# Performance work log

Hardware: AMD Instinct MI355X
Metric: run time of the kernel (lower is better)

The kernel has to match this reference:

```python
import jax, jax.numpy as jnp
import numpy as np

N_NODES = 100000
N_EDGES = 1000000
NODE_F = 128
EDGE_F = 16
HID = 64


def _layernorm(h, g, b, eps=1e-5):
    mu = jnp.mean(h, axis=-1, keepdims=True)
    var = jnp.var(h, axis=-1, keepdims=True)
    return (h - mu) * jax.lax.rsqrt(var + eps) * g + b


def _sage_conv(x, src, dst, Wl, bl, Wr):
    # PyG SAGEConv (aggr='mean'): out = lin_l(mean_{j in N(i)} x_j) + lin_r(x_i)
    agg = jax.ops.segment_sum(x[src], dst, num_segments=N_NODES)
    deg = jax.ops.segment_sum(jnp.ones((src.shape[0], 1), x.dtype), dst, num_segments=N_NODES)
    mean = agg / jnp.maximum(deg, 1.0)
    return mean @ Wl + bl + x @ Wr


def setup_inputs() -> dict:
    key = jax.random.key(0)
    ks = jax.random.split(key, 20)
    def lin(k, fi, fo):
        return jax.random.normal(k, (fi, fo), jnp.float32) / np.sqrt(fi)
    inp = {
        'x': jax.random.normal(ks[0], (N_NODES, NODE_F), jnp.float32),
        'edge_index': jax.random.randint(ks[1], (2, N_EDGES), 0, N_NODES, jnp.int32),
        'edge_attr': jax.random.normal(ks[2], (N_EDGES, EDGE_F), jnp.float32),
        # layer 0
        'Wl0': lin(ks[3], NODE_F, HID), 'bl0': jnp.zeros((HID,), jnp.float32),
        'Wr0': lin(ks[4], NODE_F, HID),
        'g0': jnp.ones((HID,), jnp.float32), 'be0': jnp.zeros((HID,), jnp.float32),
        # layer 1
        'Wl1': lin(ks[5], HID, HID), 'bl1': jnp.zeros((HID,), jnp.float32),
        'Wr1': lin(ks[6], HID, HID),
        'g1': jnp.ones((HID,), jnp.float32), 'be1': jnp.zeros((HID,), jnp.float32),
        # MLP: (2*HID+EDGE_F) -> HID -> HID//2 -> 1
        'W1': lin(ks[7], 2 * HID + EDGE_F, HID), 'b1': jnp.zeros((HID,), jnp.float32),
        'W2': lin(ks[8], HID, HID // 2), 'b2': jnp.zeros((HID // 2,), jnp.float32),
        'W3': lin(ks[9], HID // 2, 1), 'b3': jnp.zeros((1,), jnp.float32),
    }
    return inp


def reference(x, edge_index, edge_attr, Wl0, bl0, Wr0, g0, be0, Wl1, bl1, Wr1, g1, be1, W1, b1, W2, b2, W3, b3):
    src, dst = edge_index[0], edge_index[1]
    # encoder layer 0 (dropout inactive in eval)
    h = jax.nn.relu(_layernorm(_sage_conv(x, src, dst, Wl0, bl0, Wr0), g0, be0))
    # encoder layer 1
    h = jax.nn.relu(_layernorm(_sage_conv(h, src, dst, Wl1, bl1, Wr1), g1, be1))
    # edge representation: [src_emb | dst_emb | edge_attr]
    edge_repr = jnp.concatenate([h[src], h[dst], edge_attr], axis=-1)
    z = jax.nn.relu(edge_repr @ W1 + b1)
    z = jax.nn.relu(z @ W2 + b2)
    return (z @ W3 + b3).squeeze(-1)
```

## Files before the change

kernel.cpp:

```cpp
#include <hip/hip_runtime.h>
#include <hip/hip_bf16.h>

#define NN 100000
#define NE 1000000

typedef _Float16 half8  __attribute__((ext_vector_type(8)));
typedef float    f32x4  __attribute__((ext_vector_type(4)));

__device__ inline unsigned int pk2(float a, float b) {
    auto h = __builtin_amdgcn_cvt_pkrtz(a, b);
    return __builtin_bit_cast(unsigned int, h);
}
__device__ inline float f16lo(unsigned int u) {
    return (float)__builtin_bit_cast(_Float16, (unsigned short)(u & 0xffffu));
}
__device__ inline float f16hi(unsigned int u) {
    return (float)__builtin_bit_cast(_Float16, (unsigned short)(u >> 16));
}

__global__ __launch_bounds__(256) void deg_int_kernel(const int* __restrict__ dst, int* __restrict__ degi) {
    int e = blockIdx.x * 256 + threadIdx.x;
    if (e < NE) atomicAdd(&degi[dst[e]], 1);
}

__global__ __launch_bounds__(256) void scan_partial(const int* __restrict__ degi, int* __restrict__ bs) {
    __shared__ int sd[256];
    int b = blockIdx.x, t = threadIdx.x;
    int i = b * 512 + t;
    int v = (i < NN ? degi[i] : 0) + (i + 256 < NN ? degi[i + 256] : 0);
    sd[t] = v;
    __syncthreads();
    for (int o = 128; o > 0; o >>= 1) {
        if (t < o) sd[t] += sd[t + o];
        __syncthreads();
    }
    if (t == 0) bs[b] = sd[0];
}

__global__ __launch_bounds__(256) void scan_spine(const int* __restrict__ bs, int* __restrict__ bo) {
    __shared__ int sd[256];
    int t = threadIdx.x;
    int v = (t < 196) ? bs[t] : 0;
    sd[t] = v;
    __syncthreads();
    for (int o = 1; o < 256; o <<= 1) {
        int add = (t >= o) ? sd[t - o] : 0;
        __syncthreads();
        sd[t] += add;
        __syncthreads();
    }
    if (t < 196) bo[t] = sd[t] - v;
}

__global__ __launch_bounds__(512) void scan_final(const int* __restrict__ degi, const int* __restrict__ bo,
                                                  int* __restrict__ offs, int* __restrict__ cursor) {
    __shared__ int sd[512];
    int b = blockIdx.x, t = threadIdx.x;
    int i = b * 512 + t;
    int v = (i < NN) ? degi[i] : 0;
    sd[t] = v;
    __syncthreads();
    for (int o = 1; o < 512; o <<= 1) {
        int add = (t >= o) ? sd[t - o] : 0;
        __syncthreads();
        sd[t] += add;
        __syncthreads();
    }
    if (i < NN) {
        int ex = bo[b] + sd[t] - v;
        offs[i] = ex;
        cursor[i] = ex;
    }
}

__global__ __launch_bounds__(256) void csr_fill(const int* __restrict__ src, const int* __restrict__ dst,
                                                int* __restrict__ cursor, int* __restrict__ csr) {
    int e = blockIdx.x * 256 + threadIdx.x;
    if (e < NE) {
        int pos = atomicAdd(&cursor[dst[e]], 1);
        csr[pos] = src[e];
    }
}

template <int K, bool INF16>
__global__ __launch_bounds__(256, 1) void gemm_node(const void* __restrict__ inp,
                                                    const float* __restrict__ WL,
                                                    const float* __restrict__ WR,
                                                    _Float16* __restrict__ outL,
                                                    _Float16* __restrict__ outR) {
    __shared__ __align__(16) _Float16 wt[128 * K];
    __shared__ __align__(16) _Float16 at[4][16 * 136];

    int tid = threadIdx.x;
    for (int i = tid; i < K * 64; i += 256) {
        int k = i >> 6, n = i & 63;
        wt[n * K + k]        = (_Float16)WL[i];
        wt[(64 + n) * K + k] = (_Float16)WR[i];
    }
    __syncthreads();

    int wave = tid >> 6, lane = tid & 63;
    int g = lane >> 4, r = lane & 15;

    half8 bf[8][K / 32];
#pragma unroll
    for (int nt = 0; nt < 8; ++nt)
#pragma unroll
        for (int ks = 0; ks < K / 32; ++ks)
            bf[nt][ks] = *(const half8*)&wt[(nt * 16 + r) * K + ks * 32 + g * 8];

    int rowbase = blockIdx.x * 64 + wave * 16;
    int eq = lane >> 2, qq = lane & 3;
    int srow = rowbase + eq;
    if (srow > NN - 1) srow = NN - 1;
    _Float16* A = &at[wave][0];

    if constexpr (!INF16) {
        const float* sr = (const float*)inp + (size_t)srow * K + qq * (K / 4);
        unsigned int pk[K / 8];
#pragma unroll
        for (int i = 0; i < K / 16; ++i) {
            float4 v = ((const float4*)sr)[i];
            pk[2 * i]     = pk2(v.x, v.y);
            pk[2 * i + 1] = pk2(v.z, v.w);
        }
        unsigned int* da = (unsigned int*)(A + eq * 136 + qq * (K / 4));
#pragma unroll
        for (int i = 0; i < K / 32; ++i)
            ((uint4*)da)[i] = make_uint4(pk[4 * i], pk[4 * i + 1], pk[4 * i + 2], pk[4 * i + 3]);
    } else {
        const _Float16* sr = (const _Float16*)inp + (size_t)srow * K + qq * (K / 4);
        uint4* da = (uint4*)(A + eq * 136 + qq * (K / 4));
#pragma unroll
        for (int i = 0; i < K / 32; ++i)
            da[i] = ((const uint4*)sr)[i];
    }

    f32x4 acc[8];
#pragma unroll
    for (int nt = 0; nt < 8; ++nt) acc[nt] = f32x4{0.f, 0.f, 0.f, 0.f};
#pragma unroll
    for (int ks = 0; ks < K / 32; ++ks) {
        half8 af = *(const half8*)(A + r * 136 + ks * 32 + g * 8);
#pragma unroll
        for (int nt = 0; nt < 8; ++nt)
            acc[nt] = __builtin_amdgcn_mfma_f32_16x16x32_f16(af, bf[nt][ks], acc[nt], 0, 0, 0);
    }

#pragma unroll
    for (int nt = 0; nt < 8; ++nt)
#pragma unroll
        for (int rr = 0; rr < 4; ++rr)
            A[(g * 4 + rr) * 136 + nt * 16 + r] = (_Float16)acc[nt][rr];
    __syncthreads();
#pragma unroll
    for (int it = 0; it < 2; ++it) {
        int lrow = it * 8 + (lane >> 3);
        int cc = (lane & 7) * 16;
        int grow = rowbase + lrow;
        if (grow < NN) {
            uint4 u0 = *(const uint4*)&A[lrow * 136 + cc];
            uint4 u1 = *(const uint4*)&A[lrow * 136 + cc + 8];
            if (cc < 64) {
                *(uint4*)&outL[(size_t)grow * 64 + cc] = u0;
                *(uint4*)&outL[(size_t)grow * 64 + cc + 8] = u1;
            } else {
                *(uint4*)&outR[(size_t)grow * 64 + cc - 64] = u0;
                *(uint4*)&outR[(size_t)grow * 64 + cc - 56] = u1;
            }
        }
    }
}

__global__ __launch_bounds__(256) void gather_ln(const _Float16* __restrict__ vL,
                                                 const _Float16* __restrict__ pR,
                                                 const int* __restrict__ csr,
                                                 const int* __restrict__ offs,
                                                 const int* __restrict__ degi,
                                                 const float* __restrict__ bl,
                                                 const float* __restrict__ g,
                                                 const float* __restrict__ be,
                                                 _Float16* __restrict__ out) {
    int tid = threadIdx.x;
    int node = blockIdx.x * 4 + (tid >> 6);
    int lane = tid & 63;
    if (node >= NN) return;
    int h0 = lane >> 5, c = lane & 31;
    int off = offs[node], cnt = degi[node];
    float a0 = 0.f, a1 = 0.f;
    int j = 0;
    for (; j + 4 <= cnt; j += 4) {
        int r0 = csr[off + j + h0];
        int r1 = csr[off + j + 2 + h0];
        unsigned int u0 = *(const unsigned int*)&vL[(size_t)r0 * 64 + 2 * c];
        unsigned int u1 = *(const unsigned int*)&vL[(size_t)r1 * 64 + 2 * c];
        a0 += f16lo(u0); a1 += f16hi(u0);
        a0 += f16lo(u1); a1 += f16hi(u1);
    }
    for (; j + 2 <= cnt; j += 2) {
        int r0 = csr[off + j + h0];
        unsigned int u0 = *(const unsigned int*)&vL[(size_t)r0 * 64 + 2 * c];
        a0 += f16lo(u0); a1 += f16hi(u0);
    }
    if (j < cnt && h0 == 0) {
        int r0 = csr[off + j];
        unsigned int u0 = *(const unsigned int*)&vL[(size_t)r0 * 64 + 2 * c];
        a0 += f16lo(u0); a1 += f16hi(u0);
    }
    a0 += __shfl_xor(a0, 32, 64);
    a1 += __shfl_xor(a1, 32, 64);

    float dg = (float)cnt;
    dg = dg < 1.f ? 1.f : dg;
    float2 blv = *(const float2*)&bl[2 * c];
    unsigned int up = *(const unsigned int*)&pR[(size_t)node * 64 + 2 * c];
    float v0 = a0 / dg + blv.x + f16lo(up);
    float v1 = a1 / dg + blv.y + f16hi(up);
    float s = v0 + v1, s2 = v0 * v0 + v1 * v1;
#pragma unroll
    for (int o = 16; o > 0; o >>= 1) {
        s  += __shfl_xor(s, o, 64);
        s2 += __shfl_xor(s2, o, 64);
    }
    float mu = s * (1.f / 64.f);
    float var = s2 * (1.f / 64.f) - mu * mu;
    float rs = rsqrtf(var + 1e-5f);
    float2 gv  = *(const float2*)&g[2 * c];
    float2 bev = *(const float2*)&be[2 * c];
    float h0v = (v0 - mu) * rs * gv.x + bev.x;
    float h1v = (v1 - mu) * rs * gv.y + bev.y;
    h0v = h0v > 0.f ? h0v : 0.f;
    h1v = h1v > 0.f ? h1v : 0.f;
    if (h0 == 0) *(unsigned int*)&out[(size_t)node * 64 + 2 * c] = pk2(h0v, h1v);
}

#define NTILES 15625
#define ASTR 168
__global__ __launch_bounds__(256) void edge_mlp_mfma(const _Float16* __restrict__ h,
                                                     const int* __restrict__ src,
                                                     const int* __restrict__ dst,
                                                     const float* __restrict__ ea,
                                                     const float* __restrict__ W1,
                                                     const float* __restrict__ b1,
                                                     const float* __restrict__ W2,
                                                     const float* __restrict__ b2,
                                                     const float* __restrict__ W3,
                                                     const float* __restrict__ b3,
                                                     float* __restrict__ out) {
    __shared__ __align__(16) char smem[30720];
    _Float16* w1t = (_Float16*)smem;
    _Float16* w2t = (_Float16*)(smem + 20480);

    int tid = threadIdx.x;
    for (int i = tid; i < 64 * 160 / 2; i += 256) ((unsigned int*)w1t)[i] = 0u;
    __syncthreads();
    for (int i = tid; i < 144 * 64; i += 256) {
        int k = i >> 6, n = i & 63;
        w1t[n * 160 + k] = (_Float16)W1[i];
    }
    for (int i = tid; i < 64 * 32; i += 256) {
        int k = i >> 5, n = i & 31;
        w2t[n * 64 + k] = (_Float16)W2[i];
    }
    __syncthreads();

    int wave = tid >> 6;
    int lane = tid & 63;
    int g = lane >> 4;
    int r = lane & 15;

    half8 b1f[4][5];
#pragma unroll
    for (int nt = 0; nt < 4; ++nt)
#pragma unroll
        for (int ks = 0; ks < 5; ++ks)
            b1f[nt][ks] = *(const half8*)&w1t[(nt * 16 + r) * 160 + ks * 32 + g * 8];
    half8 b2f[2][2];
#pragma unroll
    for (int nt = 0; nt < 2; ++nt)
#pragma unroll
        for (int ks = 0; ks < 2; ++ks)
            b2f[nt][ks] = *(const half8*)&w2t[(nt * 16 + r) * 64 + ks * 32 + g * 8];
    __syncthreads();

    _Float16* A = (_Float16*)(smem + wave * (16 * ASTR * 2));
    _Float16* Z = (_Float16*)(smem + 4 * (16 * ASTR * 2) + wave * (16 * 72 * 2));

    float b1c0 = b1[0 * 16 + r], b1c1 = b1[1 * 16 + r], b1c2 = b1[2 * 16 + r], b1c3 = b1[3 * 16 + r];
    float b2c0 = b2[0 * 16 + r], b2c1 = b2[1 * 16 + r];
    float w3c0 = W3[0 * 16 + r], w3c1 = W3[1 * 16 + r];
    float b3v = b3[0];

    int eq = lane >> 2;
    int qq = lane & 3;

    for (int t = blockIdx.x; t < NTILES; t += gridDim.x) {
        int ebase = t * 64 + wave * 16;
        int e = ebase + eq;
        int s = src[e];
        int d = dst[e];

        const _Float16* srow = (qq < 2) ? (h + (size_t)s * 64 + qq * 32)
                                        : (h + (size_t)d * 64 + (qq - 2) * 32);
        uint4* da = (uint4*)(A + eq * ASTR + qq * 32);
#pragma unroll
        for (int i = 0; i < 4; ++i) da[i] = ((const uint4*)srow)[i];
        float4 av = *(const float4*)(ea + (size_t)e * 16 + qq * 4);
        uint2 eapk; eapk.x = pk2(av.x, av.y); eapk.y = pk2(av.z, av.w);
        *(uint2*)(A + eq * ASTR + 128 + qq * 4) = eapk;
        uint2 zz; zz.x = 0u; zz.y = 0u;
        *(uint2*)(A + eq * ASTR + 144 + qq * 4) = zz;

        f32x4 c1_0 = {b1c0, b1c0, b1c0, b1c0};
        f32x4 c1_1 = {b1c1, b1c1, b1c1, b1c1};
        f32x4 c1_2 = {b1c2, b1c2, b1c2, b1c2};
        f32x4 c1_3 = {b1c3, b1c3, b1c3, b1c3};
#pragma unroll
        for (int ks = 0; ks < 5; ++ks) {
            half8 af = *(const half8*)(A + r * ASTR + ks * 32 + g * 8);
            c1_0 = __builtin_amdgcn_mfma_f32_16x16x32_f16(af, b1f[0][ks], c1_0, 0, 0, 0);
            c1_1 = __builtin_amdgcn_mfma_f32_16x16x32_f16(af, b1f[1][ks], c1_1, 0, 0, 0);
            c1_2 = __builtin_amdgcn_mfma_f32_16x16x32_f16(af, b1f[2][ks], c1_2, 0, 0, 0);
            c1_3 = __builtin_amdgcn_mfma_f32_16x16x32_f16(af, b1f[3][ks], c1_3, 0, 0, 0);
        }
#pragma unroll
        for (int rr = 0; rr < 4; ++rr) {
            float v0 = c1_0[rr]; v0 = v0 > 0.f ? v0 : 0.f;
            float v1 = c1_1[rr]; v1 = v1 > 0.f ? v1 : 0.f;
            float v2 = c1_2[rr]; v2 = v2 > 0.f ? v2 : 0.f;
            float v3 = c1_3[rr]; v3 = v3 > 0.f ? v3 : 0.f;
            int row = g * 4 + rr;
            Z[row * 72 + 0 * 16 + r] = (_Float16)v0;
            Z[row * 72 + 1 * 16 + r] = (_Float16)v1;
            Z[row * 72 + 2 * 16 + r] = (_Float16)v2;
            Z[row * 72 + 3 * 16 + r] = (_Float16)v3;
        }

        f32x4 c2_0 = {b2c0, b2c0, b2c0, b2c0};
        f32x4 c2_1 = {b2c1, b2c1, b2c1, b2c1};
#pragma unroll
        for (int ks = 0; ks < 2; ++ks) {
            half8 a2 = *(const half8*)(Z + r * 72 + ks * 32 + g * 8);
            c2_0 = __builtin_amdgcn_mfma_f32_16x16x32_f16(a2, b2f[0][ks], c2_0, 0, 0, 0);
            c2_1 = __builtin_amdgcn_mfma_f32_16x16x32_f16(a2, b2f[1][ks], c2_1, 0, 0, 0);
        }

        float t0, t1, t2, t3;
        {
            float u0, u1;
            u0 = c2_0[0]; u0 = u0 > 0.f ? u0 : 0.f;
            u1 = c2_1[0]; u1 = u1 > 0.f ? u1 : 0.f;
            t0 = u0 * w3c0 + u1 * w3c1;
            u0 = c2_0[1]; u0 = u0 > 0.f ? u0 : 0.f;
            u1 = c2_1[1]; u1 = u1 > 0.f ? u1 : 0.f;
            t1 = u0 * w3c0 + u1 * w3c1;
            u0 = c2_0[2]; u0 = u0 > 0.f ? u0 : 0.f;
            u1 = c2_1[2]; u1 = u1 > 0.f ? u1 : 0.f;
            t2 = u0 * w3c0 + u1 * w3c1;
            u0 = c2_0[3]; u0 = u0 > 0.f ? u0 : 0.f;
            u1 = c2_1[3]; u1 = u1 > 0.f ? u1 : 0.f;
            t3 = u0 * w3c0 + u1 * w3c1;
        }
#pragma unroll
        for (int m = 1; m < 16; m <<= 1) {
            t0 += __shfl_xor(t0, m, 64);
            t1 += __shfl_xor(t1, m, 64);
            t2 += __shfl_xor(t2, m, 64);
            t3 += __shfl_xor(t3, m, 64);
        }
        if (r == 0) out[ebase + g * 4 + 0] = t0 + b3v;
        if (r == 1) out[ebase + g * 4 + 1] = t1 + b3v;
        if (r == 2) out[ebase + g * 4 + 2] = t2 + b3v;
        if (r == 3) out[ebase + g * 4 + 3] = t3 + b3v;
    }
}

#define WS_PROJL  0
#define WS_PROJR  12800000
#define WS_BUFH   25600000
#define WS_DEGI   38400000
#define WS_OFFS   38800000
#define WS_CSR    39200000
#define WS_CURS   43200000
#define WS_BSUM   43600000
#define WS_BOFF   43604096

extern "C" void kernel_launch(void* const* d_in, const int* in_sizes, int n_in,
                              void* d_out, int out_size, void* d_ws, size_t ws_size,
                              hipStream_t stream) {
    const float* x   = (const float*)d_in[0];
    const int*   ei  = (const int*)d_in[1];
    const float* ea  = (const float*)d_in[2];
    const float* Wl0 = (const float*)d_in[3];
    const float* bl0 = (const float*)d_in[4];
    const float* Wr0 = (const float*)d_in[5];
    const float* g0  = (const float*)d_in[6];
    const float* be0 = (const float*)d_in[7];
    const float* Wl1 = (const float*)d_in[8];
    const float* bl1 = (const float*)d_in[9];
    const float* Wr1 = (const float*)d_in[10];
    const float* g1  = (const float*)d_in[11];
    const float* be1 = (const float*)d_in[12];
    const float* W1  = (const float*)d_in[13];
    const float* b1  = (const float*)d_in[14];
    const float* W2  = (const float*)d_in[15];
    const float* b2  = (const float*)d_in[16];
    const float* W3  = (const float*)d_in[17];
    const float* b3  = (const float*)d_in[18];
    float* out = (float*)d_out;

    const int* src  = ei;
    const int* dstp = ei + NE;

    char* ws = (char*)d_ws;
    _Float16* projL = (_Float16*)(ws + WS_PROJL);
    _Float16* projR = (_Float16*)(ws + WS_PROJR);
    _Float16* bufH  = (_Float16*)(ws + WS_BUFH);
    int* degi   = (int*)(ws + WS_DEGI);
    int* offs   = (int*)(ws + WS_OFFS);
    int* csr    = (int*)(ws + WS_CSR);
    int* cursor = (int*)(ws + WS_CURS);
    int* bsum   = (int*)(ws + WS_BSUM);
    int* boff   = (int*)(ws + WS_BOFF);

    hipMemsetAsync(degi, 0, 400000, stream);
    deg_int_kernel<<<(NE + 255) / 256, 256, 0, stream>>>(dstp, degi);
    scan_partial<<<196, 256, 0, stream>>>(degi, bsum);
    scan_spine<<<1, 256, 0, stream>>>(bsum, boff);
    scan_final<<<196, 512, 0, stream>>>(degi, boff, offs, cursor);
    csr_fill<<<(NE + 255) / 256, 256, 0, stream>>>(src, dstp, cursor, csr);

    const int gemm_grid = (NN + 63) / 64;
    gemm_node<128, false><<<gemm_grid, 256, 0, stream>>>(x, Wl0, Wr0, projL, projR);
    gather_ln<<<NN / 4, 256, 0, stream>>>(projL, projR, csr, offs, degi, bl0, g0, be0, bufH);

    gemm_node<64, true><<<gemm_grid, 256, 0, stream>>>(bufH, Wl1, Wr1, projL, projR);
    gather_ln<<<NN / 4, 256, 0, stream>>>(projL, projR, csr, offs, degi, bl1, g1, be1, bufH);

    edge_mlp_mfma<<<3125, 256, 0, stream>>>(bufH, src, dstp, ea,
                                            W1, b1, W2, b2, W3, b3, out);
}
```

Baseline: 586.1 us.

## Load edge MLP A-fragments directly from global memory into registers

The edge MLP kernel no longer stages the concatenated [h_src | h_dst | edge_attr] tile in shared memory. Each lane now loads its MFMA A-operand fragments straight from global memory, converting edge_attr to fp16 in registers. This removes the LDS write, read round trip and its shared-memory footprint. Shared memory shrinks, the Z stride changes to 76 for bank spread, and launch bounds request 4 blocks per CU. The risk is less coalesced gathers, since 16-byte per-lane loads replace 64-byte per-lane row copies, plus register pressure from the occupancy hint.

```diff
diff --git a/kernel.cpp b/kernel.cpp
--- a/kernel.cpp
+++ b/kernel.cpp
@@ -235,19 +235,19 @@
 }
 
 #define NTILES 15625
-#define ASTR 168
-__global__ __launch_bounds__(256) void edge_mlp_mfma(const _Float16* __restrict__ h,
-                                                     const int* __restrict__ src,
-                                                     const int* __restrict__ dst,
-                                                     const float* __restrict__ ea,
-                                                     const float* __restrict__ W1,
-                                                     const float* __restrict__ b1,
-                                                     const float* __restrict__ W2,
-                                                     const float* __restrict__ b2,
-                                                     const float* __restrict__ W3,
-                                                     const float* __restrict__ b3,
-                                                     float* __restrict__ out) {
-    __shared__ __align__(16) char smem[30720];
+#define ZSTR 76
+__global__ __launch_bounds__(256, 4) void edge_mlp_mfma(const _Float16* __restrict__ h,
+                                                        const int* __restrict__ src,
+                                                        const int* __restrict__ dst,
+                                                        const float* __restrict__ ea,
+                                                        const float* __restrict__ W1,
+                                                        const float* __restrict__ b1,
+                                                        const float* __restrict__ W2,
+                                                        const float* __restrict__ b2,
+                                                        const float* __restrict__ W3,
+                                                        const float* __restrict__ b3,
+                                                        float* __restrict__ out) {
+    __shared__ __align__(16) char smem[24576];
     _Float16* w1t = (_Float16*)smem;
     _Float16* w2t = (_Float16*)(smem + 20480);
 
@@ -283,46 +283,62 @@
             b2f[nt][ks] = *(const half8*)&w2t[(nt * 16 + r) * 64 + ks * 32 + g * 8];
     __syncthreads();
 
-    _Float16* A = (_Float16*)(smem + wave * (16 * ASTR * 2));
-    _Float16* Z = (_Float16*)(smem + 4 * (16 * ASTR * 2) + wave * (16 * 72 * 2));
+    _Float16* Z = (_Float16*)(smem + wave * (16 * ZSTR * 2));
 
     float b1c0 = b1[0 * 16 + r], b1c1 = b1[1 * 16 + r], b1c2 = b1[2 * 16 + r], b1c3 = b1[3 * 16 + r];
     float b2c0 = b2[0 * 16 + r], b2c1 = b2[1 * 16 + r];
     float w3c0 = W3[0 * 16 + r], w3c1 = W3[1 * 16 + r];
     float b3v = b3[0];
 
-    int eq = lane >> 2;
-    int qq = lane & 3;
-
     for (int t = blockIdx.x; t < NTILES; t += gridDim.x) {
         int ebase = t * 64 + wave * 16;
-        int e = ebase + eq;
+        int e = ebase + r;
         int s = src[e];
         int d = dst[e];
 
-        const _Float16* srow = (qq < 2) ? (h + (size_t)s * 64 + qq * 32)
-                                        : (h + (size_t)d * 64 + (qq - 2) * 32);
-        uint4* da = (uint4*)(A + eq * ASTR + qq * 32);
-#pragma unroll
-        for (int i = 0; i < 4; ++i) da[i] = ((const uint4*)srow)[i];
-        float4 av = *(const float4*)(ea + (size_t)e * 16 + qq * 4);
-        uint2 eapk; eapk.x = pk2(av.x, av.y); eapk.y = pk2(av.z, av.w);
-        *(uint2*)(A + eq * ASTR + 128 + qq * 4) = eapk;
-        uint2 zz; zz.x = 0u; zz.y = 0u;
-        *(uint2*)(A + eq * ASTR + 144 + qq * 4) = zz;
+        const char* hs = (const char*)(h + (size_t)s * 64);
+        const char* hd = (const char*)(h + (size_t)d * 64);
+        half8 a0 = *(const half8*)(hs + g * 16);
+        half8 a1 = *(const half8*)(hs + 64 + g * 16);
+        half8 a2 = *(const half8*)(hd + g * 16);
+        half8 a3 = *(const half8*)(hd + 64 + g * 16);
+        half8 a4;
+        {
+            const float* er = ea + (size_t)e * 16 + (g & 1) * 8;
+            float4 v0 = ((const float4*)er)[0];
+            float4 v1 = ((const float4*)er)[1];
+            union { uint4 u; half8 h8; } cv;
+            cv.u = make_uint4(pk2(v0.x, v0.y), pk2(v0.z, v0.w), pk2(v1.x, v1.y), pk2(v1.z, v1.w));
+            union { uint4 u; half8 h8; } zz;
+            zz.u = make_uint4(0u, 0u, 0u, 0u);
+            a4 = (g < 2) ? cv.h8 : zz.h8;
+        }
 
         f32x4 c1_0 = {b1c0, b1c0, b1c0, b1c0};
         f32x4 c1_1 = {b1c1, b1c1, b1c1, b1c1};
         f32x4 c1_2 = {b1c2, b1c2, b1c2, b1c2};
         f32x4 c1_3 = {b1c3, b1c3, b1c3, b1c3};
-#pragma unroll
-        for (int ks = 0; ks < 5; ++ks) {
-            half8 af = *(const half8*)(A + r * ASTR + ks * 32 + g * 8);
-            c1_0 = __builtin_amdgcn_mfma_f32_16x16x32_f16(af, b1f[0][ks], c1_0, 0, 0, 0);
-            c1_1 = __builtin_amdgcn_mfma_f32_16x16x32_f16(af, b1f[1][ks], c1_1, 0, 0, 0);
-            c1_2 = __builtin_amdgcn_mfma_f32_16x16x32_f16(af, b1f[2][ks], c1_2, 0, 0, 0);
-            c1_3 = __builtin_amdgcn_mfma_f32_16x16x32_f16(af, b1f[3][ks], c1_3, 0, 0, 0);
-        }
+        c1_0 = __builtin_amdgcn_mfma_f32_16x16x32_f16(a0, b1f[0][0], c1_0, 0, 0, 0);
+        c1_1 = __builtin_amdgcn_mfma_f32_16x16x32_f16(a0, b1f[1][0], c1_1, 0, 0, 0);
+        c1_2 = __builtin_amdgcn_mfma_f32_16x16x32_f16(a0, b1f[2][0], c1_2, 0, 0, 0);
+        c1_3 = __builtin_amdgcn_mfma_f32_16x16x32_f16(a0, b1f[3][0], c1_3, 0, 0, 0);
+        c1_0 = __builtin_amdgcn_mfma_f32_16x16x32_f16(a1, b1f[0][1], c1_0, 0, 0, 0);
+        c1_1 = __builtin_amdgcn_mfma_f32_16x16x32_f16(a1, b1f[1][1], c1_1, 0, 0, 0);
+        c1_2 = __builtin_amdgcn_mfma_f32_16x16x32_f16(a1, b1f[2][1], c1_2, 0, 0, 0);
+        c1_3 = __builtin_amdgcn_mfma_f32_16x16x32_f16(a1, b1f[3][1], c1_3, 0, 0, 0);
+        c1_0 = __builtin_amdgcn_mfma_f32_16x16x32_f16(a2, b1f[0][2], c1_0, 0, 0, 0);
+        c1_1 = __builtin_amdgcn_mfma_f32_16x16x32_f16(a2, b1f[1][2], c1_1, 0, 0, 0);
+        c1_2 = __builtin_amdgcn_mfma_f32_16x16x32_f16(a2, b1f[2][2], c1_2, 0, 0, 0);
+        c1_3 = __builtin_amdgcn_mfma_f32_16x16x32_f16(a2, b1f[3][2], c1_3, 0, 0, 0);
+        c1_0 = __builtin_amdgcn_mfma_f32_16x16x32_f16(a3, b1f[0][3], c1_0, 0, 0, 0);
+        c1_1 = __builtin_amdgcn_mfma_f32_16x16x32_f16(a3, b1f[1][3], c1_1, 0, 0, 0);
+        c1_2 = __builtin_amdgcn_mfma_f32_16x16x32_f16(a3, b1f[2][3], c1_2, 0, 0, 0);
+        c1_3 = __builtin_amdgcn_mfma_f32_16x16x32_f16(a3, b1f[3][3], c1_3, 0, 0, 0);
+        c1_0 = __builtin_amdgcn_mfma_f32_16x16x32_f16(a4, b1f[0][4], c1_0, 0, 0, 0);
+        c1_1 = __builtin_amdgcn_mfma_f32_16x16x32_f16(a4, b1f[1][4], c1_1, 0, 0, 0);
+        c1_2 = __builtin_amdgcn_mfma_f32_16x16x32_f16(a4, b1f[2][4], c1_2, 0, 0, 0);
+        c1_3 = __builtin_amdgcn_mfma_f32_16x16x32_f16(a4, b1f[3][4], c1_3, 0, 0, 0);
+
 #pragma unroll
         for (int rr = 0; rr < 4; ++rr) {
             float v0 = c1_0[rr]; v0 = v0 > 0.f ? v0 : 0.f;
@@ -330,19 +346,19 @@
             float v2 = c1_2[rr]; v2 = v2 > 0.f ? v2 : 0.f;
             float v3 = c1_3[rr]; v3 = v3 > 0.f ? v3 : 0.f;
             int row = g * 4 + rr;
-            Z[row * 72 + 0 * 16 + r] = (_Float16)v0;
-            Z[row * 72 + 1 * 16 + r] = (_Float16)v1;
-            Z[row * 72 + 2 * 16 + r] = (_Float16)v2;
-            Z[row * 72 + 3 * 16 + r] = (_Float16)v3;
+            Z[row * ZSTR + 0 * 16 + r] = (_Float16)v0;
+            Z[row * ZSTR + 1 * 16 + r] = (_Float16)v1;
+            Z[row * ZSTR + 2 * 16 + r] = (_Float16)v2;
+            Z[row * ZSTR + 3 * 16 + r] = (_Float16)v3;
         }
 
         f32x4 c2_0 = {b2c0, b2c0, b2c0, b2c0};
         f32x4 c2_1 = {b2c1, b2c1, b2c1, b2c1};
 #pragma unroll
         for (int ks = 0; ks < 2; ++ks) {
-            half8 a2 = *(const half8*)(Z + r * 72 + ks * 32 + g * 8);
-            c2_0 = __builtin_amdgcn_mfma_f32_16x16x32_f16(a2, b2f[0][ks], c2_0, 0, 0, 0);
-            c2_1 = __builtin_amdgcn_mfma_f32_16x16x32_f16(a2, b2f[1][ks], c2_1, 0, 0, 0);
+            half8 a2f = *(const half8*)(Z + r * ZSTR + ks * 32 + g * 8);
+            c2_0 = __builtin_amdgcn_mfma_f32_16x16x32_f16(a2f, b2f[0][ks], c2_0, 0, 0, 0);
+            c2_1 = __builtin_amdgcn_mfma_f32_16x16x32_f16(a2f, b2f[1][ks], c2_1, 0, 0, 0);
         }
 
         float t0, t1, t2, t3;
```

New measurement: 637.5 us. 1.09x slower.
